# Kernel optimization log

Hardware: AMD Instinct MI355X
Metric: run time of the kernel (lower is better)

The kernel has to match this reference:

```python
import jax, jax.numpy as jnp
import numpy as np
from jax import lax

N_SAMPLES = 2 ** 15   # 32768
N_ATOMS = 2048
ATOM_SIZE = 1024
K_SPARSE = 64
BATCH = 4


def setup_inputs() -> dict:
    key = jax.random.key(0)
    k1, k2 = jax.random.split(key)
    orig = jax.random.normal(k1, (BATCH, 1, N_SAMPLES), dtype=jnp.float32)
    # atoms ~ uniform(-1, 1) as in the torch Parameter init
    atoms = jax.random.uniform(k2, (N_ATOMS, ATOM_SIZE), dtype=jnp.float32,
                               minval=-1.0, maxval=1.0)
    return {"orig": orig, "atoms": atoms}


def reference(orig, atoms):
    B = orig.shape[0]
    # Correlate input with the atom dictionary (F.conv1d, padding=atom_size//2).
    x = lax.conv_general_dilated(
        orig, atoms.reshape(N_ATOMS, 1, ATOM_SIZE),
        window_strides=(1,), padding=[(ATOM_SIZE // 2, ATOM_SIZE // 2)],
        dimension_numbers=("NCH", "OIH", "NCH"))  # [B, n_atoms, N+1]
    x = x[..., :N_SAMPLES]                          # [B, n_atoms, N]
    # dropout(p=0.05) omitted (eval-mode / deterministic reference)

    # sparsify: per-batch top-k over the flattened (atom, time) grid
    flat = x.reshape(B, N_ATOMS * N_SAMPLES)
    values, indices = lax.top_k(flat, K_SPARSE)      # [B, K]
    atom_idx = indices // N_SAMPLES                  # [B, K]
    time_idx = indices % N_SAMPLES                   # [B, K]

    # Overlap-add synthesis: gather atom, scale, scatter-add into 2N buffer.
    contrib = atoms[atom_idx] * values[..., None]    # [B, K, atom_size]
    pos = time_idx[..., None] + jnp.arange(ATOM_SIZE)  # [B, K, atom_size]
    b_idx = jnp.arange(B)[:, None, None]
    out = jnp.zeros((B, 2 * N_SAMPLES), dtype=orig.dtype)
    out = out.at[b_idx, pos].add(contrib)
    return out[:, None, :N_SAMPLES]                  # [B, 1, N]
```

## Files before the change

### kernel.cpp

```cpp
#include <hip/hip_runtime.h>

#define NS     32768
#define NA     2048
#define ASZ    1024
#define NB     4
#define SIGC   34848
#define BM     128
#define BN     128
#define BK     128
#define TILES  4096
#define CAP    8192
#define MINT   5080
#define SSCALE 20.0f
#define BSTR   1152
#define BSZ    18432

typedef signed char s8;
typedef __attribute__((ext_vector_type(4))) int i32x4;

__device__ __forceinline__ int imax(int a, int b) { return a > b ? a : b; }

__global__ void prep_k(const float* __restrict__ atoms, const float* __restrict__ orig,
                       s8* __restrict__ apack, s8* __restrict__ sigsh,
                       float* __restrict__ sigf, int* __restrict__ wlc) {
  if (blockIdx.x == 0 && threadIdx.x == 0) *wlc = 0;
  if (blockIdx.x < 1024) {
    int g = blockIdx.x >> 3, kt = blockIdx.x & 7;
    int t = threadIdx.x;
    int kk = t >> 7, r = t & 127, l = r >> 1, half = r & 1;
    int row = g * 16 + (l & 15);
    int kbase = kt * 128 + (kk * 4 + (l >> 4)) * 16 + half * 8;
    const float* srow = atoms + (size_t)row * ASZ + kbase;
    s8* dst = apack + (size_t)(((g * 8 + kt) * 2 + kk) << 10) + l * 16 + half * 8;
    #pragma unroll
    for (int j = 0; j < 8; j++) {
      float q = fminf(127.f, fmaxf(-127.f, srow[j] * 127.f));
      dst[j] = (s8)__float2int_rn(q);
    }
  } else {
    int r = blockIdx.x - 1024;
    int nch = (SIGC + 255) / 256;
    int bm = r / nch, chunk = r % nch;
    int i = chunk * 256 + threadIdx.x;
    if (i >= SIGC) return;
    int b = bm >> 4, m = bm & 15;
    int j = i + m - 512;
    float f = (j >= 0 && j < NS) ? orig[(size_t)b * NS + j] : 0.0f;
    float q = fminf(127.f, fmaxf(-127.f, f * SSCALE));
    sigsh[(size_t)bm * SIGC + i] = (s8)__float2int_rn(q);
    if (m == 0) sigf[(size_t)b * SIGC + i] = f;
  }
}

__device__ __forceinline__ void stage_bsig(const s8* __restrict__ Sb, int t0,
                                           s8* Bsig, int w, int lane) {
  #pragma unroll
  for (int i = 0; i < 5; i++) {
    int c = w + 4 * i;
    if (c < 18) {
      int o = c * 1024 + lane * 16;
      int m = o / BSTR;
      int pp = (o - m * BSTR) >> 4;
      int s = (pp & ~7) | ((pp ^ m) & 7);
      const s8* src = Sb + (size_t)m * SIGC + t0 + (s << 4);
      __builtin_amdgcn_global_load_lds((const __attribute__((address_space(1))) void*)src,
          (__attribute__((address_space(3))) void*)(&Bsig[c * 1024]), 16, 0, 0);
    }
  }
}

__device__ __forceinline__ void compute_tile(const s8* __restrict__ Apk, const s8* Bsig, int kt,
                                             int w, int lane, i32x4 acc[4][4]) {
  int wr = w >> 1, wc = w & 1;
  int kgrp = lane >> 4;
  int m = lane & 15, mx = m & 7;
  const s8* brow = Bsig + m * BSTR;
  const s8* abase = Apk + ((((size_t)wr * 4 * 8 + kt) * 2) << 10) + (lane << 4);
  int sb = wc * 4 + kgrp + kt * 8;
  #pragma unroll
  for (int kk = 0; kk < 2; kk++) {
    i32x4 af[4], bfr[4];
    #pragma unroll
    for (int mf = 0; mf < 4; mf++)
      af[mf] = *(const i32x4*)&abase[((mf * 16 + kk) << 10)];
    #pragma unroll
    for (int nf = 0; nf < 4; nf++) {
      int s = sb + nf + kk * 4;
      int ps = (s & ~7) | ((s ^ mx) & 7);
      bfr[nf] = *(const i32x4*)&brow[ps << 4];
    }
    __builtin_amdgcn_s_setprio(1);
    #pragma unroll
    for (int mf = 0; mf < 4; mf++)
      #pragma unroll
      for (int nf = 0; nf < 4; nf++)
        acc[mf][nf] = __builtin_amdgcn_mfma_i32_16x16x64_i8(af[mf], bfr[nf], acc[mf][nf], 0, 0, 0);
    __builtin_amdgcn_s_setprio(0);
  }
}

#define K_LOOP(Apk, Sb, t0)                                   \
  stage_bsig(Sb, t0, Bsig, w, lane);                          \
  __syncthreads();                                            \
  _Pragma("unroll 2")                                         \
  for (int kt = 0; kt < 8; kt++)                              \
    compute_tile(Apk, Bsig, kt, w, lane, acc);

__global__ __launch_bounds__(256, 4)
void screen1(const s8* __restrict__ apack, const s8* __restrict__ sigsh,
             int* __restrict__ tmax)
{
  __shared__ __align__(16) s8 Bsig[BSZ];
  __shared__ int wred[4];
  int bid0 = blockIdx.x;
  int bid  = (bid0 & 7) * ((NB * TILES) >> 3) + (bid0 >> 3);
  int b = bid >> 12, tile = bid & 4095;
  int mt = tile >> 8, nt = tile & 255;
  int m0 = mt * BM, t0 = nt * BN;
  int tid = threadIdx.x, w = tid >> 6, lane = tid & 63;
  const s8* Apk = apack + (size_t)mt * 131072;
  const s8* Sb = sigsh + (size_t)b * 16 * SIGC;

  i32x4 acc[4][4];
  #pragma unroll
  for (int i = 0; i < 4; i++)
    #pragma unroll
    for (int j = 0; j < 4; j++) acc[i][j] = (i32x4){0, 0, 0, 0};

  K_LOOP(Apk, Sb, t0)

  int lmax = -2147483647;
  #pragma unroll
  for (int mf = 0; mf < 4; mf++)
    #pragma unroll
    for (int nf = 0; nf < 4; nf++)
      #pragma unroll
      for (int q = 0; q < 4; q++) lmax = imax(lmax, acc[mf][nf][q]);
  #pragma unroll
  for (int off = 32; off; off >>= 1) lmax = imax(lmax, __shfl_xor(lmax, off, 64));
  if (lane == 0) wred[w] = lmax;
  __syncthreads();
  if (tid == 0)
    tmax[b * TILES + tile] = imax(imax(wred[0], wred[1]), imax(wred[2], wred[3]));
}

__global__ void thresh_k(const int* __restrict__ tmax, int* __restrict__ thr,
                         int* __restrict__ ccnt, int* __restrict__ wl, int* __restrict__ wlc) {
  int b = blockIdx.x, tid = threadIdx.x;
  __shared__ int hist[4096];
  __shared__ int tsum[256];
  __shared__ int hist2[256];
  __shared__ int sB1, sAbove, sThr;
  for (int i = tid; i < 4096; i += 256) hist[i] = 0;
  __syncthreads();
  for (int i = tid; i < TILES; i += 256) {
    unsigned u = (unsigned)tmax[b * TILES + i] ^ 0x80000000u;
    atomicAdd(&hist[u >> 20], 1);
  }
  __syncthreads();
  { int s = 0;
    for (int j = 0; j < 16; j++) s += hist[tid * 16 + j];
    tsum[tid] = s; }
  __syncthreads();
  if (tid == 0) {
    int cum = 0, T = 0;
    for (int t2 = 255; t2 >= 0; t2--) {
      if (cum + tsum[t2] >= 64) { T = t2; break; }
      cum += tsum[t2];
    }
    int B1 = T * 16;
    for (int bk = T * 16 + 15; bk >= T * 16; bk--) {
      if (cum + hist[bk] >= 64) { B1 = bk; break; }
      cum += hist[bk];
    }
    sB1 = B1; sAbove = cum;
  }
  __syncthreads();
  if (tid < 256) hist2[tid] = 0;
  __syncthreads();
  int B1 = sB1;
  for (int i = tid; i < TILES; i += 256) {
    unsigned u = (unsigned)tmax[b * TILES + i] ^ 0x80000000u;
    if ((int)(u >> 20) == B1) atomicAdd(&hist2[(u >> 12) & 255], 1);
  }
  __syncthreads();
  if (tid == 0) {
    int cum = sAbove, B2 = 0;
    for (int z = 255; z >= 0; z--) { cum += hist2[z]; if (cum >= 64) { B2 = z; break; } }
    unsigned ulow = ((unsigned)B1 << 20) | ((unsigned)B2 << 12);
    int t = (int)(ulow ^ 0x80000000u);
    sThr = t; thr[b] = t; ccnt[b] = 0;
  }
  __syncthreads();
  int cut = sThr - MINT;
  for (int i = tid; i < TILES; i += 256)
    if (tmax[b * TILES + i] >= cut) { int p = atomicAdd(wlc, 1); wl[p] = (b << 12) | i; }
}

__global__ __launch_bounds__(256, 4)
void screen2(const s8* __restrict__ apack, const s8* __restrict__ sigsh,
             const int* __restrict__ thr, const int* __restrict__ wl,
             const int* __restrict__ wlc, int* __restrict__ ccnt, int* __restrict__ cidx)
{
  __shared__ __align__(16) s8 Bsig[BSZ];
  int n = *wlc; if (n > NB * TILES) n = NB * TILES;
  int tid = threadIdx.x, w = tid >> 6, lane = tid & 63;
  int wr = w >> 1, wc = w & 1;
  int kgrp = lane >> 4;

  for (int wi = blockIdx.x; wi < n; wi += gridDim.x) {
    int e = wl[wi];
    int b = e >> 12, tile = e & 4095;
    int cut = thr[b] - MINT;
    int mt = tile >> 8, nt = tile & 255;
    int m0 = mt * BM, t0 = nt * BN;
    const s8* Apk = apack + (size_t)mt * 131072;
    const s8* Sb = sigsh + (size_t)b * 16 * SIGC;

    i32x4 acc[4][4];
    #pragma unroll
    for (int i = 0; i < 4; i++)
      #pragma unroll
      for (int j = 0; j < 4; j++) acc[i][j] = (i32x4){0, 0, 0, 0};

    K_LOOP(Apk, Sb, t0)

    int rb = m0 + wr * 64 + 4 * kgrp;
    int cb = t0 + wc * 64 + (lane & 15);
    #pragma unroll
    for (int mf = 0; mf < 4; mf++)
      #pragma unroll
      for (int nf = 0; nf < 4; nf++)
        #pragma unroll
        for (int q = 0; q < 4; q++) {
          if (acc[mf][nf][q] >= cut) {
            int a = rb + mf * 16 + q;
            int t = cb + nf * 16;
            int p = atomicAdd(&ccnt[b], 1);
            if (p < CAP) cidx[b * CAP + p] = (a << 15) | t;
          }
        }
    __syncthreads();
  }
}

__global__ void rescore_k(const float* __restrict__ atoms, const float* __restrict__ sigf,
                          const int* __restrict__ ccnt, const int* __restrict__ cidx,
                          float* __restrict__ cval) {
  int nwv = gridDim.x * 4;
  int gw = blockIdx.x * 4 + (threadIdx.x >> 6);
  int lane = threadIdx.x & 63;
  for (int b = 0; b < NB; b++) {
    int cnt = ccnt[b]; if (cnt > CAP) cnt = CAP;
    for (int ci = gw; ci < cnt; ci += nwv) {
      int idx = cidx[b * CAP + ci];
      int a = idx >> 15, t = idx & (NS - 1);
      const float* ap = atoms + (size_t)a * ASZ;
      const float* sp = sigf + (size_t)b * SIGC + t;
      float sum = 0.f;
      #pragma unroll
      for (int j = 0; j < 16; j++) { int k = lane + 64 * j; sum += ap[k] * sp[k]; }
      #pragma unroll
      for (int off = 32; off; off >>= 1) sum += __shfl_xor(sum, off, 64);
      if (lane == 0) cval[b * CAP + ci] = sum;
    }
  }
}

__global__ void select_k(const int* __restrict__ ccnt, const float* __restrict__ cval,
                         const int* __restrict__ cidx, float* __restrict__ sval,
                         int* __restrict__ sidx) {
  int b = blockIdx.x, tid = threadIdx.x;
  int cnt = ccnt[b]; if (cnt > CAP) cnt = CAP;
  __shared__ float lv[2048];
  __shared__ int li[2048];
  for (int ii = 0; ii * 256 < cnt; ii++) {
    int i = ii * 256 + tid;
    float vi = 0.f; int idi = 0; bool act = i < cnt;
    if (act) { vi = cval[b * CAP + i]; idi = cidx[b * CAP + i]; }
    int rank = 0;
    for (int c0 = 0; c0 < cnt; c0 += 2048) {
      int mchunk = cnt - c0; if (mchunk > 2048) mchunk = 2048;
      __syncthreads();
      for (int j = tid; j < mchunk; j += 256) {
        lv[j] = cval[b * CAP + c0 + j];
        li[j] = cidx[b * CAP + c0 + j];
      }
      __syncthreads();
      if (act)
        for (int j = 0; j < mchunk; j++)
          rank += (lv[j] > vi) || (lv[j] == vi && li[j] < idi);
    }
    if (act && rank < 64) { sval[b * 64 + rank] = vi; sidx[b * 64 + rank] = idi; }
  }
}

__global__ void recon_k(const float* __restrict__ atoms, const float* __restrict__ sval,
                        const int* __restrict__ sidx, float* __restrict__ out) {
  int gp = blockIdx.x * 256 + threadIdx.x;
  int b = gp >> 15, p = gp & (NS - 1);
  __shared__ float vv[64];
  __shared__ int ii[64];
  if (threadIdx.x < 64) {
    vv[threadIdx.x] = sval[b * 64 + threadIdx.x];
    ii[threadIdx.x] = sidx[b * 64 + threadIdx.x];
  }
  __syncthreads();
  float acc = 0.f;
  for (int s = 0; s < 64; s++) {
    int idx = ii[s];
    int a = idx >> 15, t = idx & (NS - 1);
    int off = p - t;
    if (off >= 0 && off < ASZ) acc += vv[s] * atoms[(size_t)a * ASZ + off];
  }
  out[gp] = acc;
}

extern "C" void kernel_launch(void* const* d_in, const int* in_sizes, int n_in,
                              void* d_out, int out_size, void* d_ws, size_t ws_size,
                              hipStream_t stream) {
  const float* orig  = (const float*)d_in[0];
  const float* atoms = (const float*)d_in[1];
  float* out = (float*)d_out;
  char* ws = (char*)d_ws;

  s8*    apack = (s8*)   (ws + 0);
  s8*    sigsh = (s8*)   (ws + 2097152);
  float* sigf  = (float*)(ws + 4327424);
  int*   tmax  = (int*)  (ws + 4884992);
  int*   thr   = (int*)  (ws + 4950528);
  int*   ccnt  = (int*)  (ws + 4950784);
  float* cval  = (float*)(ws + 4951040);
  int*   cidx  = (int*)  (ws + 5082112);
  float* sval  = (float*)(ws + 5213184);
  int*   sidx  = (int*)  (ws + 5214208);
  int*   wl    = (int*)  (ws + 5215232);
  int*   wlc   = (int*)  (ws + 5280768);

  int nch = (SIGC + 255) / 256;
  prep_k<<<1024 + NB * 16 * nch, 256, 0, stream>>>(atoms, orig, apack, sigsh, sigf, wlc);
  screen1<<<NB * TILES, 256, 0, stream>>>(apack, sigsh, tmax);
  thresh_k<<<NB, 256, 0, stream>>>(tmax, thr, ccnt, wl, wlc);
  screen2<<<512, 256, 0, stream>>>(apack, sigsh, thr, wl, wlc, ccnt, cidx);
  rescore_k<<<128, 256, 0, stream>>>(atoms, sigf, ccnt, cidx, cval);
  select_k<<<NB, 256, 0, stream>>>(ccnt, cval, cidx, sval, sidx);
  recon_k<<<out_size / 256, 256, 0, stream>>>(atoms, sval, sidx, out);
}
```

Measured before the change: 282.4 us.

## Switch int8 screening GEMM from 16x16x64 to 32x32x32 MFMA tiles

```diff
diff --git a/kernel.cpp b/kernel.cpp
--- a/kernel.cpp
+++ b/kernel.cpp
@@ -17,6 +17,7 @@
 
 typedef signed char s8;
 typedef __attribute__((ext_vector_type(4))) int i32x4;
+typedef __attribute__((ext_vector_type(16))) int i32x16;
 
 __device__ __forceinline__ int imax(int a, int b) { return a > b ? a : b; }
 
@@ -24,21 +25,21 @@
                        s8* __restrict__ apack, s8* __restrict__ sigsh,
                        float* __restrict__ sigf, int* __restrict__ wlc) {
   if (blockIdx.x == 0 && threadIdx.x == 0) *wlc = 0;
-  if (blockIdx.x < 1024) {
+  if (blockIdx.x < 512) {
     int g = blockIdx.x >> 3, kt = blockIdx.x & 7;
     int t = threadIdx.x;
-    int kk = t >> 7, r = t & 127, l = r >> 1, half = r & 1;
-    int row = g * 16 + (l & 15);
-    int kbase = kt * 128 + (kk * 4 + (l >> 4)) * 16 + half * 8;
-    const float* srow = atoms + (size_t)row * ASZ + kbase;
-    s8* dst = apack + (size_t)(((g * 8 + kt) * 2 + kk) << 10) + l * 16 + half * 8;
-    #pragma unroll
-    for (int j = 0; j < 8; j++) {
+    int ks = t >> 6, l = t & 63;
+    int row = g * 32 + (l & 31);
+    int kcol = kt * 128 + ks * 32 + 16 * (l >> 5);
+    const float* srow = atoms + (size_t)row * ASZ + kcol;
+    s8* dst = apack + ((size_t)((g * 8 + kt) * 4 + ks) << 10) + l * 16;
+    #pragma unroll
+    for (int j = 0; j < 16; j++) {
       float q = fminf(127.f, fmaxf(-127.f, srow[j] * 127.f));
       dst[j] = (s8)__float2int_rn(q);
     }
   } else {
-    int r = blockIdx.x - 1024;
+    int r = blockIdx.x - 512;
     int nch = (SIGC + 255) / 256;
     int bm = r / nch, chunk = r % nch;
     int i = chunk * 256 + threadIdx.x;
@@ -70,31 +71,31 @@
 }
 
 __device__ __forceinline__ void compute_tile(const s8* __restrict__ Apk, const s8* Bsig, int kt,
-                                             int w, int lane, i32x4 acc[4][4]) {
+                                             int w, int lane, i32x16 acc[2][2]) {
   int wr = w >> 1, wc = w & 1;
-  int kgrp = lane >> 4;
+  int kg = lane >> 5;
   int m = lane & 15, mx = m & 7;
   const s8* brow = Bsig + m * BSTR;
-  const s8* abase = Apk + ((((size_t)wr * 4 * 8 + kt) * 2) << 10) + (lane << 4);
-  int sb = wc * 4 + kgrp + kt * 8;
-  #pragma unroll
-  for (int kk = 0; kk < 2; kk++) {
-    i32x4 af[4], bfr[4];
-    #pragma unroll
-    for (int mf = 0; mf < 4; mf++)
-      af[mf] = *(const i32x4*)&abase[((mf * 16 + kk) << 10)];
-    #pragma unroll
-    for (int nf = 0; nf < 4; nf++) {
-      int s = sb + nf + kk * 4;
+  int sbase = wc * 4 + ((lane >> 4) & 1) + kt * 8 + kg;
+  const s8* abase = Apk + ((size_t)(((wr * 2) * 8 + kt) * 4) << 10) + (lane << 4);
+  #pragma unroll
+  for (int ks = 0; ks < 4; ks++) {
+    i32x4 af[2], bfr[2];
+    #pragma unroll
+    for (int mf = 0; mf < 2; mf++)
+      af[mf] = *(const i32x4*)&abase[((size_t)(mf * 32 + ks) << 10)];
+    #pragma unroll
+    for (int nf = 0; nf < 2; nf++) {
+      int s = sbase + nf * 2 + ks * 2;
       int ps = (s & ~7) | ((s ^ mx) & 7);
       bfr[nf] = *(const i32x4*)&brow[ps << 4];
     }
     __builtin_amdgcn_s_setprio(1);
     #pragma unroll
-    for (int mf = 0; mf < 4; mf++)
-      #pragma unroll
-      for (int nf = 0; nf < 4; nf++)
-        acc[mf][nf] = __builtin_amdgcn_mfma_i32_16x16x64_i8(af[mf], bfr[nf], acc[mf][nf], 0, 0, 0);
+    for (int mf = 0; mf < 2; mf++)
+      #pragma unroll
+      for (int nf = 0; nf < 2; nf++)
+        acc[mf][nf] = __builtin_amdgcn_mfma_i32_32x32x32_i8(af[mf], bfr[nf], acc[mf][nf], 0, 0, 0);
     __builtin_amdgcn_s_setprio(0);
   }
 }
@@ -104,7 +105,7 @@
   __syncthreads();                                            \
   _Pragma("unroll 2")                                         \
   for (int kt = 0; kt < 8; kt++)                              \
-    compute_tile(Apk, Bsig, kt, w, lane, acc);
+    compute_tile(Apk, Sb##sig, kt, w, lane, acc);
 
 __global__ __launch_bounds__(256, 4)
 void screen1(const s8* __restrict__ apack, const s8* __restrict__ sigsh,
@@ -121,21 +122,27 @@
   const s8* Apk = apack + (size_t)mt * 131072;
   const s8* Sb = sigsh + (size_t)b * 16 * SIGC;
 
-  i32x4 acc[4][4];
-  #pragma unroll
-  for (int i = 0; i < 4; i++)
-    #pragma unroll
-    for (int j = 0; j < 4; j++) acc[i][j] = (i32x4){0, 0, 0, 0};
-
-  K_LOOP(Apk, Sb, t0)
+  i32x16 acc[2][2];
+  #pragma unroll
+  for (int i = 0; i < 2; i++)
+    #pragma unroll
+    for (int j = 0; j < 2; j++)
+      #pragma unroll
+      for (int q = 0; q < 16; q++) acc[i][j][q] = 0;
+
+  stage_bsig(Sb, t0, Bsig, w, lane);
+  __syncthreads();
+  #pragma unroll 2
+  for (int kt = 0; kt < 8; kt++)
+    compute_tile(Apk, Bsig, kt, w, lane, acc);
 
   int lmax = -2147483647;
   #pragma unroll
-  for (int mf = 0; mf < 4; mf++)
-    #pragma unroll
-    for (int nf = 0; nf < 4; nf++)
-      #pragma unroll
-      for (int q = 0; q < 4; q++) lmax = imax(lmax, acc[mf][nf][q]);
+  for (int mf = 0; mf < 2; mf++)
+    #pragma unroll
+    for (int nf = 0; nf < 2; nf++)
+      #pragma unroll
+      for (int q = 0; q < 16; q++) lmax = imax(lmax, acc[mf][nf][q]);
   #pragma unroll
   for (int off = 32; off; off >>= 1) lmax = imax(lmax, __shfl_xor(lmax, off, 64));
   if (lane == 0) wred[w] = lmax;
@@ -206,7 +213,6 @@
   int n = *wlc; if (n > NB * TILES) n = NB * TILES;
   int tid = threadIdx.x, w = tid >> 6, lane = tid & 63;
   int wr = w >> 1, wc = w & 1;
-  int kgrp = lane >> 4;
 
   for (int wi = blockIdx.x; wi < n; wi += gridDim.x) {
     int e = wl[wi];
@@ -217,25 +223,31 @@
     const s8* Apk = apack + (size_t)mt * 131072;
     const s8* Sb = sigsh + (size_t)b * 16 * SIGC;
 
-    i32x4 acc[4][4];
-    #pragma unroll
-    for (int i = 0; i < 4; i++)
-      #pragma unroll
-      for (int j = 0; j < 4; j++) acc[i][j] = (i32x4){0, 0, 0, 0};
-
-    K_LOOP(Apk, Sb, t0)
-
-    int rb = m0 + wr * 64 + 4 * kgrp;
-    int cb = t0 + wc * 64 + (lane & 15);
-    #pragma unroll
-    for (int mf = 0; mf < 4; mf++)
-      #pragma unroll
-      for (int nf = 0; nf < 4; nf++)
+    i32x16 acc[2][2];
+    #pragma unroll
+    for (int i = 0; i < 2; i++)
+      #pragma unroll
+      for (int j = 0; j < 2; j++)
         #pragma unroll
-        for (int q = 0; q < 4; q++) {
+        for (int q = 0; q < 16; q++) acc[i][j][q] = 0;
+
+    stage_bsig(Sb, t0, Bsig, w, lane);
+    __syncthreads();
+    #pragma unroll 2
+    for (int kt = 0; kt < 8; kt++)
+      compute_tile(Apk, Bsig, kt, w, lane, acc);
+
+    int rb = m0 + wr * 64 + 4 * (lane >> 5);
+    int cb = t0 + wc * 64 + (lane & 31);
+    #pragma unroll
+    for (int mf = 0; mf < 2; mf++)
+      #pragma unroll
+      for (int nf = 0; nf < 2; nf++)
+        #pragma unroll
+        for (int q = 0; q < 16; q++) {
           if (acc[mf][nf][q] >= cut) {
-            int a = rb + mf * 16 + q;
-            int t = cb + nf * 16;
+            int a = rb + mf * 32 + (q & 3) + 8 * (q >> 2);
+            int t = cb + nf * 32;
             int p = atomicAdd(&ccnt[b], 1);
             if (p < CAP) cidx[b * CAP + p] = (a << 15) | t;
           }
@@ -338,7 +350,7 @@
   int*   wlc   = (int*)  (ws + 5280768);
 
   int nch = (SIGC + 255) / 256;
-  prep_k<<<1024 + NB * 16 * nch, 256, 0, stream>>>(atoms, orig, apack, sigsh, sigf, wlc);
+  prep_k<<<512 + NB * 16 * nch, 256, 0, stream>>>(atoms, orig, apack, sigsh, sigf, wlc);
   screen1<<<NB * TILES, 256, 0, stream>>>(apack, sigsh, tmax);
   thresh_k<<<NB, 256, 0, stream>>>(tmax, thr, ccnt, wl, wlc);
   screen2<<<512, 256, 0, stream>>>(apack, sigsh, thr, wl, wlc, ccnt, cidx);
```

After: 326.8 us. 1.16x slower.
